# Kernel tuning notes

Hardware: AMD Instinct MI355X
Metric: run time of the kernel (lower is better)

Reference implementation:

```python
import jax, jax.numpy as jnp
import numpy as np
import math

N, E = 1000, 128000
IN_DIM, HID, OUT_DIM = 256, 512, 16
L, H = 6, 8
C = HID // H  # 64, TransformerConv out_channels per head
EDGE_DIM = 32
MAX_LEN = 1000


def _pe(max_len, d_model):
    pos = np.arange(max_len)[:, None].astype(np.float32)
    div = np.exp(np.arange(0, d_model, 2).astype(np.float32) * (-math.log(10000.0) / d_model))
    pe = np.zeros((max_len, d_model), dtype=np.float32)
    pe[:, 0::2] = np.sin(pos * div)
    pe[:, 1::2] = np.cos(pos * div)
    return jnp.asarray(pe)


def setup_inputs() -> dict:
    key = jax.random.key(0)
    ks = jax.random.split(key, 32)
    g = lambda k, shape, fan_in: jax.random.normal(k, shape, jnp.float32) / jnp.sqrt(jnp.float32(fan_in))
    inp = {
        "x": jax.random.normal(ks[0], (N, IN_DIM), jnp.float32),
        "edge_index": jax.random.randint(ks[1], (2, E), 0, N, jnp.int64 if jax.config.jax_enable_x64 else jnp.int32),
        "edge_attr": jax.random.uniform(ks[2], (E, 4), jnp.float32),
        "embed_w": g(ks[3], (IN_DIM, HID), IN_DIM),
        "embed_b": jnp.zeros((HID,), jnp.float32),
        "pe": _pe(MAX_LEN, HID),
        "ee_w1": g(ks[4], (4, 16), 4), "ee_b1": jnp.zeros((16,), jnp.float32),
        "ee_w2": g(ks[5], (16, EDGE_DIM), 16), "ee_b2": jnp.zeros((EDGE_DIM,), jnp.float32),
        "q_w": g(ks[6], (L, HID, HID), HID), "q_b": jnp.zeros((L, HID), jnp.float32),
        "k_w": g(ks[7], (L, HID, HID), HID), "k_b": jnp.zeros((L, HID), jnp.float32),
        "v_w": g(ks[8], (L, HID, HID), HID), "v_b": jnp.zeros((L, HID), jnp.float32),
        "e_w": g(ks[9], (L, EDGE_DIM, HID), EDGE_DIM),
        "skip_w": g(ks[10], (L, HID, HID), HID), "skip_b": jnp.zeros((L, HID), jnp.float32),
        "ln_g": jnp.ones((L, HID), jnp.float32), "ln_b": jnp.zeros((L, HID), jnp.float32),
        "dom_w": g(ks[11], (HID, 16), HID), "dom_b": jnp.zeros((16,), jnp.float32),
        "cls_w1": g(ks[12], (HID + 16, HID // 2), HID + 16), "cls_b1": jnp.zeros((HID // 2,), jnp.float32),
        "cls_w2": g(ks[13], (HID // 2, OUT_DIM), HID // 2), "cls_b2": jnp.zeros((OUT_DIM,), jnp.float32),
    }
    return inp


def _layer_norm(x, g, b, eps=1e-5):
    mu = jnp.mean(x, axis=-1, keepdims=True)
    var = jnp.var(x, axis=-1, keepdims=True)
    return (x - mu) * jax.lax.rsqrt(var + eps) * g + b


def _forward(x, edge_index, edge_attr, embed_w, embed_b, pe, ee_w1, ee_b1, ee_w2, ee_b2,
             q_w, q_b, k_w, k_b, v_w, v_b, e_w, skip_w, skip_b, ln_g, ln_b,
             dom_w, dom_b, cls_w1, cls_b1, cls_w2, cls_b2):
    n = x.shape[0]
    h = x @ embed_w + embed_b
    h = h + pe[:n]
    # edge encoder: 4 -> 16 -> 32
    ef = jax.nn.relu(edge_attr @ ee_w1 + ee_b1) @ ee_w2 + ee_b2  # [E, 32]
    src, tgt = edge_index[0], edge_index[1]
    scale = 1.0 / math.sqrt(C)
    for l in range(L):
        res = h
        q = (h @ q_w[l] + q_b[l]).reshape(n, H, C)
        k = (h @ k_w[l] + k_b[l]).reshape(n, H, C)
        v = (h @ v_w[l] + v_b[l]).reshape(n, H, C)
        e = (ef @ e_w[l]).reshape(-1, H, C)            # [E, H, C], lin_edge has no bias
        kj = k[src] + e                                 # gather + edge bias
        score = jnp.sum(q[tgt] * kj, axis=-1) * scale   # [E, H]
        # segment softmax over incoming edges of each target node
        m = jax.ops.segment_max(score, tgt, num_segments=n)     # [N, H]
        al = jnp.exp(score - m[tgt])
        den = jax.ops.segment_sum(al, tgt, num_segments=n)      # [N, H]
        al = al / den[tgt]
        msg = (v[src] + e) * al[:, :, None]             # [E, H, C]
        out = jax.ops.segment_sum(msg, tgt, num_segments=n).reshape(n, HID)
        out = out + h @ skip_w[l] + skip_b[l]           # root_weight skip
        h = _layer_norm(out + res, ln_g[l], ln_b[l])
    dom = h @ dom_w + dom_b                             # [N, 16]
    comb = jnp.concatenate([h, dom], axis=-1)
    hid = jax.nn.relu(comb @ cls_w1 + cls_b1)
    return hid @ cls_w2 + cls_b2


def reference(x, edge_index, edge_attr, embed_w, embed_b, pe, ee_w1, ee_b1, ee_w2, ee_b2,
              q_w, q_b, k_w, k_b, v_w, v_b, e_w, skip_w, skip_b, ln_g, ln_b,
              dom_w, dom_b, cls_w1, cls_b1, cls_w2, cls_b2):
    return _forward(x, edge_index, edge_attr, embed_w, embed_b, pe, ee_w1, ee_b1, ee_w2, ee_b2,
                    q_w, q_b, k_w, k_b, v_w, v_b, e_w, skip_w, skip_b, ln_g, ln_b,
                    dom_w, dom_b, cls_w1, cls_b1, cls_w2, cls_b2)
```

## Files before the change

kernel.cpp:

```cpp
#include <hip/hip_runtime.h>
#include <hip/hip_bf16.h>
#include <cstdint>
#include <cstddef>

#define NN 1000
#define EE 128000
#define LAYERS 6
#define SCALE 0.125f
#define MAXDEG 320

typedef __attribute__((ext_vector_type(4))) float f32x4;
typedef __attribute__((ext_vector_type(8))) short short8v;

static __device__ __forceinline__ unsigned short f2bf(float x){
    unsigned int u = __float_as_uint(x);
    unsigned int lsb = (u >> 16) & 1u;
    u += 0x7fffu + lsb;
    return (unsigned short)(u >> 16);
}
static __device__ __forceinline__ float bf2f(unsigned short u){
    return __uint_as_float(((unsigned int)u) << 16);
}

__global__ void zero_counts(int* cnt){
    cnt[threadIdx.x] = 0;
}

__global__ void hist_kernel(const int* __restrict__ tgt, int* cnt){
    int e = blockIdx.x*256 + threadIdx.x;
    if (e < EE) atomicAdd(&cnt[tgt[e]], 1);
}

__global__ void scan_kernel(const int* __restrict__ cnt, int* offs, int* cursor){
    __shared__ int s[1024];
    int tid = threadIdx.x;
    s[tid] = (tid < NN) ? cnt[tid] : 0;
    __syncthreads();
    for (int st = 1; st < 1024; st <<= 1){
        int v = (tid >= st) ? s[tid-st] : 0;
        __syncthreads();
        s[tid] += v;
        __syncthreads();
    }
    int excl = (tid == 0) ? 0 : s[tid-1];
    if (tid < NN){ offs[tid] = excl; cursor[tid] = excl; }
    if (tid == 0) offs[NN] = s[NN-1];
}

__global__ void scatter_kernel(const int* __restrict__ src, const int* __restrict__ tgt,
                               int* cursor, int* ssrc, int* epos){
    int e = blockIdx.x*256 + threadIdx.x;
    if (e < EE){
        int t = tgt[e];
        int pos = atomicAdd(&cursor[t], 1);
        ssrc[pos] = src[e];
        epos[e] = pos;
    }
}

__global__ __launch_bounds__(256) void edge_enc(
    const float* __restrict__ edge_attr,
    const float* __restrict__ w1, const float* __restrict__ b1,
    const float* __restrict__ w2, const float* __restrict__ b2,
    const int* __restrict__ epos,
    unsigned short* __restrict__ efs)
{
    __shared__ float w1s[64], b1s[16], w2s[512], b2s[32];
    int tid = threadIdx.x;
    if (tid < 64) w1s[tid] = w1[tid];
    if (tid < 16) b1s[tid] = b1[tid];
    if (tid < 32) b2s[tid] = b2[tid];
    w2s[tid] = w2[tid];
    w2s[tid+256] = w2[tid+256];
    __syncthreads();
    int e = blockIdx.x*256 + tid;
    if (e >= EE) return;
    float4 av = *(const float4*)(edge_attr + (size_t)e*4);
    float hd[16];
    #pragma unroll
    for (int i = 0; i < 16; i++){
        float v = av.x*w1s[i] + av.y*w1s[16+i] + av.z*w1s[32+i] + av.w*w1s[48+i] + b1s[i];
        hd[i] = fmaxf(v, 0.f);
    }
    unsigned short* op = efs + (size_t)epos[e]*32;
    #pragma unroll
    for (int k4 = 0; k4 < 8; k4++){
        ushort4 ub;
        float v0 = b2s[k4*4+0], v1 = b2s[k4*4+1], v2 = b2s[k4*4+2], v3 = b2s[k4*4+3];
        #pragma unroll
        for (int i = 0; i < 16; i++){
            float hv = hd[i];
            v0 += hv*w2s[i*32 + k4*4+0];
            v1 += hv*w2s[i*32 + k4*4+1];
            v2 += hv*w2s[i*32 + k4*4+2];
            v3 += hv*w2s[i*32 + k4*4+3];
        }
        ub.x = f2bf(v0); ub.y = f2bf(v1); ub.z = f2bf(v2); ub.w = f2bf(v3);
        *(ushort4*)(op + k4*4) = ub;
    }
}

__global__ __launch_bounds__(256) void convert_x(const float* __restrict__ x, unsigned short* __restrict__ xb){
    int row = blockIdx.x;
    int c = threadIdx.x;
    xb[(size_t)row*256 + c] = (row < NN) ? f2bf(x[(size_t)row*256 + c]) : (unsigned short)0;
}

__global__ __launch_bounds__(256) void tconv(const float* __restrict__ src, unsigned short* __restrict__ dst,
                                             int Kk, int Nn){
    int tn = blockIdx.x, tk = blockIdx.y;
    __shared__ float ts[32][33];
    int tid = threadIdx.x;
    int r = tid >> 3, c0 = (tid & 7)*4;
    float4 v = *(const float4*)(src + (size_t)(tk*32 + r)*Nn + tn*32 + c0);
    ts[r][c0+0] = v.x; ts[r][c0+1] = v.y; ts[r][c0+2] = v.z; ts[r][c0+3] = v.w;
    __syncthreads();
    ushort4 o;
    o.x = f2bf(ts[c0+0][r]); o.y = f2bf(ts[c0+1][r]);
    o.z = f2bf(ts[c0+2][r]); o.w = f2bf(ts[c0+3][r]);
    *(ushort4*)(dst + (size_t)(tn*32 + r)*Kk + tk*32 + c0) = o;
}

__global__ __launch_bounds__(256) void tconv24(
    const float* __restrict__ Wq, const float* __restrict__ Wk,
    const float* __restrict__ Wv, const float* __restrict__ Ws,
    unsigned short* __restrict__ Wt)
{
    int bid = blockIdx.x;
    int mm = bid >> 8;
    int tile = bid & 255;
    int tk = tile >> 4, tn = tile & 15;
    int l = mm >> 2, m = mm & 3;
    const float* W = ((m==0)?Wq:(m==1)?Wk:(m==2)?Wv:Ws) + (size_t)l*512*512;
    unsigned short* dst = Wt + (size_t)mm*512*512;
    __shared__ float ts[32][33];
    int tid = threadIdx.x;
    int r = tid >> 3, c0 = (tid & 7)*4;
    float4 v = *(const float4*)(W + (size_t)(tk*32 + r)*512 + tn*32 + c0);
    ts[r][c0+0] = v.x; ts[r][c0+1] = v.y; ts[r][c0+2] = v.z; ts[r][c0+3] = v.w;
    __syncthreads();
    ushort4 o;
    o.x = f2bf(ts[c0+0][r]); o.y = f2bf(ts[c0+1][r]);
    o.z = f2bf(ts[c0+2][r]); o.w = f2bf(ts[c0+3][r]);
    *(ushort4*)(dst + (size_t)(tn*32 + r)*512 + tk*32 + c0) = o;
}

__global__ __launch_bounds__(256) void gemm_embed_mfma(
    const unsigned short* __restrict__ xb,
    const unsigned short* __restrict__ ewt,
    const float* __restrict__ bias, const float* __restrict__ pe,
    float* __restrict__ C, unsigned short* __restrict__ hb)
{
    int bid = blockIdx.x;
    int mt = bid >> 2, nt = bid & 3;
    int row0 = mt*64, col0 = nt*128;

    __shared__ __align__(16) unsigned short As[64*40];
    __shared__ __align__(16) unsigned short Bs[128*40];

    int tid = threadIdx.x;
    int wid = tid >> 6, l = tid & 63;
    int wm = wid >> 1, wn = wid & 1;

    f32x4 acc[2][4] = {};
    int ar = tid >> 2, akq = tid & 3;
    for (int k0 = 0; k0 < 256; k0 += 32){
        *(uint4*)&As[ar*40 + akq*8]      = *(const uint4*)&xb[(size_t)(row0+ar)*256 + k0 + akq*8];
        *(uint4*)&Bs[ar*40 + akq*8]      = *(const uint4*)&ewt[(size_t)(col0+ar)*256 + k0 + akq*8];
        *(uint4*)&Bs[(ar+64)*40 + akq*8] = *(const uint4*)&ewt[(size_t)(col0+ar+64)*256 + k0 + akq*8];
        __syncthreads();
        short8v a0 = *(const short8v*)&As[(wm*32 + (l&15))*40 + (l>>4)*8];
        short8v a1 = *(const short8v*)&As[(wm*32 + 16 + (l&15))*40 + (l>>4)*8];
        #pragma unroll
        for (int nj = 0; nj < 4; nj++){
            short8v b = *(const short8v*)&Bs[(wn*64 + nj*16 + (l&15))*40 + (l>>4)*8];
            acc[0][nj] = __builtin_amdgcn_mfma_f32_16x16x32_bf16(a0, b, acc[0][nj], 0, 0, 0);
            acc[1][nj] = __builtin_amdgcn_mfma_f32_16x16x32_bf16(a1, b, acc[1][nj], 0, 0, 0);
        }
        __syncthreads();
    }
    int rbase = (l >> 4)*4, cl = l & 15;
    #pragma unroll
    for (int mi = 0; mi < 2; mi++)
        #pragma unroll
        for (int nj = 0; nj < 4; nj++)
            #pragma unroll
            for (int r = 0; r < 4; r++){
                int grow = row0 + wm*32 + mi*16 + rbase + r;
                int gcol = col0 + wn*64 + nj*16 + cl;
                if (grow < NN){
                    float v = acc[mi][nj][r] + bias[gcol] + pe[(size_t)grow*512 + gcol];
                    C[(size_t)grow*512 + gcol] = v;
                    hb[(size_t)grow*512 + gcol] = f2bf(v);
                }
            }
}

__global__ __launch_bounds__(256) void gemm_qkvs_mfma(
    const unsigned short* __restrict__ hb,
    const unsigned short* __restrict__ Wt,
    const float* __restrict__ qb, const float* __restrict__ kb,
    const float* __restrict__ vb, const float* __restrict__ sb,
    float* __restrict__ Q, unsigned short* __restrict__ K16,
    unsigned short* __restrict__ V16, float* __restrict__ S)
{
    int bid = blockIdx.x;
    int mat = bid >> 7;
    int rem = bid & 127;
    int mt = rem >> 3, nt = rem & 7;
    int row0 = mt*64, col0 = nt*64;
    const unsigned short* W = Wt + (size_t)mat*512*512;
    const float* bias = (mat==0)?qb:(mat==1)?kb:(mat==2)?vb:sb;

    __shared__ __align__(16) unsigned short As[64*72];
    __shared__ __align__(16) unsigned short Bs[64*72];

    int tid = threadIdx.x;
    int wid = tid >> 6, l = tid & 63;
    int wm = wid >> 1, wn = wid & 1;

    f32x4 acc[2][2] = {};
    int lr = tid >> 2;
    int lc = (tid & 3)*2;
    const unsigned short* ga = hb + (size_t)(row0+lr)*512 + lc*8;
    const unsigned short* gb = W  + (size_t)(col0+lr)*512 + lc*8;

    uint4 ra0 = *(const uint4*)(ga);
    uint4 ra1 = *(const uint4*)(ga + 8);
    uint4 rb0 = *(const uint4*)(gb);
    uint4 rb1 = *(const uint4*)(gb + 8);

    for (int k0 = 0; k0 < 512; k0 += 64){
        __syncthreads();
        *(uint4*)&As[lr*72 + lc*8]     = ra0;
        *(uint4*)&As[lr*72 + lc*8 + 8] = ra1;
        *(uint4*)&Bs[lr*72 + lc*8]     = rb0;
        *(uint4*)&Bs[lr*72 + lc*8 + 8] = rb1;
        __syncthreads();
        if (k0 + 64 < 512){
            ra0 = *(const uint4*)(ga + k0 + 64);
            ra1 = *(const uint4*)(ga + k0 + 72);
            rb0 = *(const uint4*)(gb + k0 + 64);
            rb1 = *(const uint4*)(gb + k0 + 72);
        }
        #pragma unroll
        for (int ks = 0; ks < 2; ks++){
            short8v a0 = *(const short8v*)&As[(wm*32 + (l&15))*72      + ks*32 + (l>>4)*8];
            short8v a1 = *(const short8v*)&As[(wm*32 + 16 + (l&15))*72 + ks*32 + (l>>4)*8];
            short8v b0 = *(const short8v*)&Bs[(wn*32 + (l&15))*72      + ks*32 + (l>>4)*8];
            short8v b1 = *(const short8v*)&Bs[(wn*32 + 16 + (l&15))*72 + ks*32 + (l>>4)*8];
            acc[0][0] = __builtin_amdgcn_mfma_f32_16x16x32_bf16(a0, b0, acc[0][0], 0, 0, 0);
            acc[0][1] = __builtin_amdgcn_mfma_f32_16x16x32_bf16(a0, b1, acc[0][1], 0, 0, 0);
            acc[1][0] = __builtin_amdgcn_mfma_f32_16x16x32_bf16(a1, b0, acc[1][0], 0, 0, 0);
            acc[1][1] = __builtin_amdgcn_mfma_f32_16x16x32_bf16(a1, b1, acc[1][1], 0, 0, 0);
        }
    }
    int rbase = (l >> 4)*4, cl = l & 15;
    #pragma unroll
    for (int mi = 0; mi < 2; mi++)
        #pragma unroll
        for (int nj = 0; nj < 2; nj++)
            #pragma unroll
            for (int r = 0; r < 4; r++){
                int grow = row0 + wm*32 + mi*16 + rbase + r;
                int gcol = col0 + wn*32 + nj*16 + cl;
                if (grow < NN){
                    float v = acc[mi][nj][r] + bias[gcol];
                    if (mat == 0)      Q[(size_t)grow*512 + gcol] = v;
                    else if (mat == 1) K16[(size_t)grow*512 + gcol] = f2bf(v);
                    else if (mat == 2) V16[(size_t)grow*512 + gcol] = f2bf(v);
                    else               S[(size_t)grow*512 + gcol] = v;
                }
            }
}

__global__ __launch_bounds__(512) void attn_layer(
    const float* __restrict__ hcur,
    const float* __restrict__ Qm, const unsigned short* __restrict__ Km,
    const unsigned short* __restrict__ Vm, const float* __restrict__ SKm,
    const unsigned short* __restrict__ efs, const float* __restrict__ e_w_l,
    const float* __restrict__ ln_g_l, const float* __restrict__ ln_b_l,
    const int* __restrict__ ssrc, const int* __restrict__ offs,
    float* __restrict__ hnext, unsigned short* __restrict__ hbn)
{
    int tid = threadIdx.x;
    int t = blockIdx.x;

    __shared__ float q_s[8*68];
    __shared__ float qe_s[8*36];
    __shared__ float sc_s[MAXDEG*8];
    __shared__ int   src_s[MAXDEG];
    __shared__ float pv_s[2048];
    __shared__ float pe_s[512];
    __shared__ float s_s[256];
    __shared__ float red[64], red2[64];
    __shared__ float m_s[8], d_s[8];

    q_s[(tid>>6)*68 + (tid&63)] = Qm[(size_t)t*512 + tid];
    __syncthreads();
    if (tid < 256){
        int hh = tid>>5, dd = tid&31;
        const float* wrow = e_w_l + (size_t)dd*512 + hh*64;
        const float* qh = q_s + hh*68;
        float a = 0.f;
        #pragma unroll
        for (int c = 0; c < 64; c++) a += qh[c]*wrow[c];
        qe_s[hh*36 + dd] = a;
    }
    int start = offs[t], deg = offs[t+1] - start;
    __syncthreads();

    int cw = tid >> 5, l = tid & 31;
    int h = l >> 2, sub = l & 3;
    const float4* qp4  = (const float4*)(q_s + h*68 + sub*16);
    const float4* qep4 = (const float4*)(qe_s + h*36 + sub*8);
    float4 qa0 = qp4[0], qa1 = qp4[1], qa2 = qp4[2], qa3 = qp4[3];
    float4 qe0 = qep4[0], qe1 = qep4[1];
    float lmax = -1e30f;
    for (int i = cw; i < deg; i += 16){
        int s = ssrc[start + i];
        if (l == 0) src_s[i] = s;
        const unsigned short* kr = Km + (size_t)s*512 + l*16;
        short8v k0 = *(const short8v*)(kr);
        short8v k1 = *(const short8v*)(kr + 8);
        short8v ev = *(const short8v*)(efs + (size_t)(start+i)*32 + sub*8);
        float p;
        p  = qa0.x*bf2f((unsigned short)k0[0]) + qa0.y*bf2f((unsigned short)k0[1])
           + qa0.z*bf2f((unsigned short)k0[2]) + qa0.w*bf2f((unsigned short)k0[3]);
        p += qa1.x*bf2f((unsigned short)k0[4]) + qa1.y*bf2f((unsigned short)k0[5])
           + qa1.z*bf2f((unsigned short)k0[6]) + qa1.w*bf2f((unsigned short)k0[7]);
        p += qa2.x*bf2f((unsigned short)k1[0]) + qa2.y*bf2f((unsigned short)k1[1])
           + qa2.z*bf2f((unsigned short)k1[2]) + qa2.w*bf2f((unsigned short)k1[3]);
        p += qa3.x*bf2f((unsigned short)k1[4]) + qa3.y*bf2f((unsigned short)k1[5])
           + qa3.z*bf2f((unsigned short)k1[6]) + qa3.w*bf2f((unsigned short)k1[7]);
        p += qe0.x*bf2f((unsigned short)ev[0]) + qe0.y*bf2f((unsigned short)ev[1])
           + qe0.z*bf2f((unsigned short)ev[2]) + qe0.w*bf2f((unsigned short)ev[3]);
        p += qe1.x*bf2f((unsigned short)ev[4]) + qe1.y*bf2f((unsigned short)ev[5])
           + qe1.z*bf2f((unsigned short)ev[6]) + qe1.w*bf2f((unsigned short)ev[7]);
        p += __shfl_xor(p, 1);
        p += __shfl_xor(p, 2);
        p *= SCALE;
        lmax = fmaxf(lmax, p);
        if (sub == 0) sc_s[i*8 + h] = p;
    }
    lmax = fmaxf(lmax, __shfl_xor(lmax, 32));
    if (((tid & 63) < 32) && sub == 0) red[(tid>>6)*8 + h] = lmax;
    __syncthreads();
    if (tid < 8){
        float m = red[tid];
        #pragma unroll
        for (int w = 1; w < 8; w++) m = fmaxf(m, red[w*8 + tid]);
        m_s[tid] = m;
    }
    __syncthreads();

    {
        int he = tid & 7, ie = tid >> 3;
        float mh = m_s[he];
        float den = 0.f;
        for (int i = ie; i < deg; i += 64){
            float al = __expf(sc_s[i*8 + he] - mh);
            sc_s[i*8 + he] = al;
            den += al;
        }
        den += __shfl_xor(den, 8);
        den += __shfl_xor(den, 16);
        den += __shfl_xor(den, 32);
        if ((tid & 63) < 8) red2[(tid>>6)*8 + (tid & 7)] = den;
    }
    __syncthreads();
    if (tid < 8){
        float d = 0.f;
        #pragma unroll
        for (int w = 0; w < 8; w++) d += red2[w*8 + tid];
        d_s[tid] = d;
    }
    __syncthreads();

    {
        int c4 = tid & 127, g = tid >> 7;
        int h2 = c4 >> 4;
        float4 acc = make_float4(0.f, 0.f, 0.f, 0.f);
        #pragma unroll 4
        for (int i = g; i < deg; i += 4){
            int s = src_s[i];
            float al = sc_s[i*8 + h2];
            ushort4 v = *(const ushort4*)(Vm + (size_t)s*512 + c4*4);
            acc.x += al*bf2f(v.x); acc.y += al*bf2f(v.y);
            acc.z += al*bf2f(v.z); acc.w += al*bf2f(v.w);
        }
        *(float4*)&pv_s[g*512 + c4*4] = acc;
    }
    {
        int c2 = tid & 255, g2 = tid >> 8;
        int h3 = c2 >> 5, dd3 = c2 & 31;
        float accE = 0.f;
        #pragma unroll 8
        for (int i = g2; i < deg; i += 2){
            float al = sc_s[i*8 + h3];
            accE += al * bf2f(efs[(size_t)(start+i)*32 + dd3]);
        }
        pe_s[g2*256 + c2] = accE;
    }
    __syncthreads();
    if (tid < 256){
        float dv = d_s[tid>>5];
        float invd = (dv > 0.f) ? 1.f/dv : 0.f;
        s_s[tid] = (pe_s[tid] + pe_s[256+tid]) * invd;
    }
    __syncthreads();

    int c = tid;
    int hh2 = c >> 6;
    float dv = d_s[hh2];
    float invd = (dv > 0.f) ? 1.f/dv : 0.f;
    float vtot = pv_s[c] + pv_s[512+c] + pv_s[1024+c] + pv_s[1536+c];
    float r = vtot * invd;
    float oe = 0.f;
    const float* sp = s_s + hh2*32;
    #pragma unroll
    for (int d = 0; d < 32; d++) oe += sp[d]*e_w_l[(size_t)d*512 + c];
    float x = r + oe + SKm[(size_t)t*512 + c] + hcur[(size_t)t*512 + c];

    int wv = tid >> 6, ln = tid & 63;
    float sA = x, sB = x*x;
    #pragma unroll
    for (int m2 = 1; m2 <= 32; m2 <<= 1){
        sA += __shfl_xor(sA, m2);
        sB += __shfl_xor(sB, m2);
    }
    if (ln == 0){ red[wv] = sA; red2[wv] = sB; }
    __syncthreads();
    float tot = 0.f, tot2 = 0.f;
    #pragma unroll
    for (int w = 0; w < 8; w++){ tot += red[w]; tot2 += red2[w]; }
    float mu  = tot*(1.f/512.f);
    float var = tot2*(1.f/512.f) - mu*mu;
    float rstd = rsqrtf(var + 1e-5f);
    float y = (x - mu)*rstd*ln_g_l[c] + ln_b_l[c];
    hnext[(size_t)t*512 + c] = y;
    hbn[(size_t)t*512 + c]   = f2bf(y);
}

__global__ __launch_bounds__(256) void final_head(
    const float* __restrict__ hin,
    const float* __restrict__ dom_w, const float* __restrict__ dom_b,
    const float* __restrict__ w1, const float* __restrict__ b1,
    const float* __restrict__ w2, const float* __restrict__ b2,
    float* __restrict__ out)
{
    int tid = threadIdx.x, t = blockIdx.x;
    __shared__ float h_s[512];
    __shared__ float dom_s[16];
    __shared__ float hid_s[256];
    __shared__ float red[256];
    h_s[tid]     = hin[(size_t)t*512 + tid];
    h_s[tid+256] = hin[(size_t)t*512 + 256 + tid];
    __syncthreads();
    if (tid < 16){
        float a = dom_b[tid];
        for (int i = 0; i < 512; i++) a += h_s[i]*dom_w[i*16 + tid];
        dom_s[tid] = a;
    }
    __syncthreads();
    float acc = b1[tid];
    for (int i = 0; i < 512; i++) acc += h_s[i]*w1[(size_t)i*256 + tid];
    #pragma unroll
    for (int i = 0; i < 16; i++) acc += dom_s[i]*w1[(size_t)(512+i)*256 + tid];
    hid_s[tid] = fmaxf(acc, 0.f);
    __syncthreads();
    int o = tid & 15, g = tid >> 4;
    float p = 0.f;
    #pragma unroll
    for (int j = 0; j < 16; j++) p += hid_s[g*16 + j]*w2[(g*16 + j)*16 + o];
    red[tid] = p;
    __syncthreads();
    if (tid < 16){
        float s2 = b2[tid];
        for (int gg = 0; gg < 16; gg++) s2 += red[gg*16 + tid];
        out[(size_t)t*16 + tid] = s2;
    }
}

extern "C" void kernel_launch(void* const* d_in, const int* in_sizes, int n_in,
                              void* d_out, int out_size, void* d_ws, size_t ws_size,
                              hipStream_t stream)
{
    const float* x       = (const float*)d_in[0];
    const int*   eidx    = (const int*)  d_in[1];
    const float* eattr   = (const float*)d_in[2];
    const float* embed_w = (const float*)d_in[3];
    const float* embed_b = (const float*)d_in[4];
    const float* pe      = (const float*)d_in[5];
    const float* ee_w1   = (const float*)d_in[6];
    const float* ee_b1   = (const float*)d_in[7];
    const float* ee_w2   = (const float*)d_in[8];
    const float* ee_b2   = (const float*)d_in[9];
    const float* q_w     = (const float*)d_in[10];
    const float* q_b     = (const float*)d_in[11];
    const float* k_w     = (const float*)d_in[12];
    const float* k_b     = (const float*)d_in[13];
    const float* v_w     = (const float*)d_in[14];
    const float* v_b     = (const float*)d_in[15];
    const float* e_w     = (const float*)d_in[16];
    const float* skip_w  = (const float*)d_in[17];
    const float* skip_b  = (const float*)d_in[18];
    const float* ln_g    = (const float*)d_in[19];
    const float* ln_b    = (const float*)d_in[20];
    const float* dom_w   = (const float*)d_in[21];
    const float* dom_b   = (const float*)d_in[22];
    const float* cls_w1  = (const float*)d_in[23];
    const float* cls_b1  = (const float*)d_in[24];
    const float* cls_w2  = (const float*)d_in[25];
    const float* cls_b2  = (const float*)d_in[26];
    float* out = (float*)d_out;

    float* ws = (float*)d_ws;
    size_t o = 0;
    float* h0    = ws + o; o += (size_t)512*NN;
    float* h1    = ws + o; o += (size_t)512*NN;
    float* Qb    = ws + o; o += (size_t)512*NN;
    float* Sb    = ws + o; o += (size_t)512*NN;
    unsigned short* Kb16 = (unsigned short*)(ws + o); o += (size_t)1024*512/2;
    unsigned short* Vb16 = (unsigned short*)(ws + o); o += (size_t)1024*512/2;
    unsigned short* efs  = (unsigned short*)(ws + o); o += (size_t)EE*32/2;
    unsigned short* hb   = (unsigned short*)(ws + o); o += (size_t)1024*512/2;
    unsigned short* xb   = (unsigned short*)(ws + o); o += (size_t)1024*256/2;
    unsigned short* ewt  = (unsigned short*)(ws + o); o += (size_t)512*256/2;
    unsigned short* Wtb  = (unsigned short*)(ws + o); o += (size_t)24*512*512/2;
    int* cnt    = (int*)(ws + o); o += 1024;
    int* offs   = (int*)(ws + o); o += 1024;
    int* cursor = (int*)(ws + o); o += 1024;
    int* ssrc   = (int*)(ws + o); o += EE;
    int* epos   = (int*)(ws + o); o += EE;

    const int* srcp = eidx;
    const int* tgtp = eidx + EE;

    zero_counts<<<1, 1024, 0, stream>>>(cnt);
    hist_kernel<<<EE/256, 256, 0, stream>>>(tgtp, cnt);
    scan_kernel<<<1, 1024, 0, stream>>>(cnt, offs, cursor);
    scatter_kernel<<<EE/256, 256, 0, stream>>>(srcp, tgtp, cursor, ssrc, epos);
    edge_enc<<<EE/256, 256, 0, stream>>>(eattr, ee_w1, ee_b1, ee_w2, ee_b2, epos, efs);
    convert_x<<<1024, 256, 0, stream>>>(x, xb);
    tconv<<<dim3(512/32, 256/32), 256, 0, stream>>>(embed_w, ewt, 256, 512);
    tconv24<<<24*256, 256, 0, stream>>>(q_w, k_w, v_w, skip_w, Wtb);
    gemm_embed_mfma<<<64, 256, 0, stream>>>(xb, ewt, embed_b, pe, h0, hb);

    float* hc = h0;
    float* hn = h1;
    for (int l = 0; l < LAYERS; l++){
        gemm_qkvs_mfma<<<512, 256, 0, stream>>>(
            hb, Wtb + (size_t)l*4*512*512,
            q_b + (size_t)l*512, k_b + (size_t)l*512,
            v_b + (size_t)l*512, skip_b + (size_t)l*512,
            Qb, Kb16, Vb16, Sb);
        attn_layer<<<NN, 512, 0, stream>>>(
            hc, Qb, Kb16, Vb16, Sb, efs, e_w + (size_t)l*32*512,
            ln_g + (size_t)l*512, ln_b + (size_t)l*512,
            ssrc, offs, hn, hb);
        float* tmp = hc; hc = hn; hn = tmp;
    }
    final_head<<<NN, 256, 0, stream>>>(hc, dom_w, dom_b, cls_w1, cls_b1, cls_w2, cls_b2, out);
}
```

Baseline: 581.1 us.

## Split attention per node across two head-group blocks and fuse weight conversions

```diff
diff --git a/kernel.cpp b/kernel.cpp
--- a/kernel.cpp
+++ b/kernel.cpp
@@ -100,49 +100,47 @@
     }
 }
 
-__global__ __launch_bounds__(256) void convert_x(const float* __restrict__ x, unsigned short* __restrict__ xb){
-    int row = blockIdx.x;
-    int c = threadIdx.x;
-    xb[(size_t)row*256 + c] = (row < NN) ? f2bf(x[(size_t)row*256 + c]) : (unsigned short)0;
-}
-
-__global__ __launch_bounds__(256) void tconv(const float* __restrict__ src, unsigned short* __restrict__ dst,
-                                             int Kk, int Nn){
-    int tn = blockIdx.x, tk = blockIdx.y;
-    __shared__ float ts[32][33];
-    int tid = threadIdx.x;
-    int r = tid >> 3, c0 = (tid & 7)*4;
-    float4 v = *(const float4*)(src + (size_t)(tk*32 + r)*Nn + tn*32 + c0);
-    ts[r][c0+0] = v.x; ts[r][c0+1] = v.y; ts[r][c0+2] = v.z; ts[r][c0+3] = v.w;
-    __syncthreads();
-    ushort4 o;
-    o.x = f2bf(ts[c0+0][r]); o.y = f2bf(ts[c0+1][r]);
-    o.z = f2bf(ts[c0+2][r]); o.w = f2bf(ts[c0+3][r]);
-    *(ushort4*)(dst + (size_t)(tn*32 + r)*Kk + tk*32 + c0) = o;
-}
-
-__global__ __launch_bounds__(256) void tconv24(
+__global__ __launch_bounds__(256) void convert_all(
     const float* __restrict__ Wq, const float* __restrict__ Wk,
     const float* __restrict__ Wv, const float* __restrict__ Ws,
-    unsigned short* __restrict__ Wt)
+    const float* __restrict__ embed_w, const float* __restrict__ x,
+    unsigned short* __restrict__ Wt, unsigned short* __restrict__ ewt,
+    unsigned short* __restrict__ xb)
 {
     int bid = blockIdx.x;
-    int mm = bid >> 8;
-    int tile = bid & 255;
-    int tk = tile >> 4, tn = tile & 15;
-    int l = mm >> 2, m = mm & 3;
-    const float* W = ((m==0)?Wq:(m==1)?Wk:(m==2)?Wv:Ws) + (size_t)l*512*512;
-    unsigned short* dst = Wt + (size_t)mm*512*512;
-    __shared__ float ts[32][33];
     int tid = threadIdx.x;
-    int r = tid >> 3, c0 = (tid & 7)*4;
-    float4 v = *(const float4*)(W + (size_t)(tk*32 + r)*512 + tn*32 + c0);
-    ts[r][c0+0] = v.x; ts[r][c0+1] = v.y; ts[r][c0+2] = v.z; ts[r][c0+3] = v.w;
-    __syncthreads();
-    ushort4 o;
-    o.x = f2bf(ts[c0+0][r]); o.y = f2bf(ts[c0+1][r]);
-    o.z = f2bf(ts[c0+2][r]); o.w = f2bf(ts[c0+3][r]);
-    *(ushort4*)(dst + (size_t)(tn*32 + r)*512 + tk*32 + c0) = o;
+    if (bid < 6144){
+        int mm = bid >> 8;
+        int tile = bid & 255;
+        int tk = tile >> 4, tn = tile & 15;
+        int l = mm >> 2, m = mm & 3;
+        const float* W = ((m==0)?Wq:(m==1)?Wk:(m==2)?Wv:Ws) + (size_t)l*512*512;
+        unsigned short* dst = Wt + (size_t)mm*512*512;
+        __shared__ float ts[32][33];
+        int r = tid >> 3, c0 = (tid & 7)*4;
+        float4 v = *(const float4*)(W + (size_t)(tk*32 + r)*512 + tn*32 + c0);
+        ts[r][c0+0] = v.x; ts[r][c0+1] = v.y; ts[r][c0+2] = v.z; ts[r][c0+3] = v.w;
+        __syncthreads();
+        ushort4 o;
+        o.x = f2bf(ts[c0+0][r]); o.y = f2bf(ts[c0+1][r]);
+        o.z = f2bf(ts[c0+2][r]); o.w = f2bf(ts[c0+3][r]);
+        *(ushort4*)(dst + (size_t)(tn*32 + r)*512 + tk*32 + c0) = o;
+    } else if (bid < 6144 + 128){
+        int tile = bid - 6144;
+        int tn = tile & 15, tk = tile >> 4;
+        __shared__ float ts2[32][33];
+        int r = tid >> 3, c0 = (tid & 7)*4;
+        float4 v = *(const float4*)(embed_w + (size_t)(tk*32 + r)*512 + tn*32 + c0);
+        ts2[r][c0+0] = v.x; ts2[r][c0+1] = v.y; ts2[r][c0+2] = v.z; ts2[r][c0+3] = v.w;
+        __syncthreads();
+        ushort4 o;
+        o.x = f2bf(ts2[c0+0][r]); o.y = f2bf(ts2[c0+1][r]);
+        o.z = f2bf(ts2[c0+2][r]); o.w = f2bf(ts2[c0+3][r]);
+        *(ushort4*)(ewt + (size_t)(tn*32 + r)*256 + tk*32 + c0) = o;
+    } else {
+        int row = bid - 6144 - 128;
+        xb[(size_t)row*256 + tid] = (row < NN) ? f2bf(x[(size_t)row*256 + tid]) : (unsigned short)0;
+    }
 }
 
 __global__ __launch_bounds__(256) void gemm_embed_mfma(
@@ -274,172 +272,174 @@
             }
 }
 
-__global__ __launch_bounds__(512) void attn_layer(
-    const float* __restrict__ hcur,
+__global__ __launch_bounds__(256) void attn_h4(
     const float* __restrict__ Qm, const unsigned short* __restrict__ Km,
-    const unsigned short* __restrict__ Vm, const float* __restrict__ SKm,
+    const unsigned short* __restrict__ Vm,
     const unsigned short* __restrict__ efs, const float* __restrict__ e_w_l,
-    const float* __restrict__ ln_g_l, const float* __restrict__ ln_b_l,
     const int* __restrict__ ssrc, const int* __restrict__ offs,
-    float* __restrict__ hnext, unsigned short* __restrict__ hbn)
+    float* __restrict__ x_pre)
 {
     int tid = threadIdx.x;
-    int t = blockIdx.x;
-
-    __shared__ float q_s[8*68];
-    __shared__ float qe_s[8*36];
-    __shared__ float sc_s[MAXDEG*8];
+    int b = blockIdx.x;
+    int t = b >> 1;
+    int hh0 = (b & 1)*4;
+
+    __shared__ float q_s[4*68];
+    __shared__ float qe_s[4*36];
+    __shared__ float sc_s[MAXDEG*4];
     __shared__ int   src_s[MAXDEG];
-    __shared__ float pv_s[2048];
-    __shared__ float pe_s[512];
-    __shared__ float s_s[256];
-    __shared__ float red[64], red2[64];
-    __shared__ float m_s[8], d_s[8];
-
-    q_s[(tid>>6)*68 + (tid&63)] = Qm[(size_t)t*512 + tid];
-    __syncthreads();
-    if (tid < 256){
-        int hh = tid>>5, dd = tid&31;
-        const float* wrow = e_w_l + (size_t)dd*512 + hh*64;
-        const float* qh = q_s + hh*68;
+    __shared__ float pv_s[4*256];
+    __shared__ float pe_s[4*128];
+    __shared__ float s_s[128];
+    __shared__ float red[16], red2[16];
+    __shared__ float m_s[4], d_s[4];
+
+    q_s[(tid>>6)*68 + (tid&63)] = Qm[(size_t)t*512 + hh0*64 + tid];
+    __syncthreads();
+    if (tid < 128){
+        int h = tid >> 5, d = tid & 31;
+        const float* wrow = e_w_l + (size_t)d*512 + (hh0+h)*64;
+        const float* qh = q_s + h*68;
         float a = 0.f;
         #pragma unroll
         for (int c = 0; c < 64; c++) a += qh[c]*wrow[c];
-        qe_s[hh*36 + dd] = a;
+        qe_s[h*36 + d] = a;
     }
     int start = offs[t], deg = offs[t+1] - start;
     __syncthreads();
 
     int cw = tid >> 5, l = tid & 31;
-    int h = l >> 2, sub = l & 3;
-    const float4* qp4  = (const float4*)(q_s + h*68 + sub*16);
-    const float4* qep4 = (const float4*)(qe_s + h*36 + sub*8);
-    float4 qa0 = qp4[0], qa1 = qp4[1], qa2 = qp4[2], qa3 = qp4[3];
-    float4 qe0 = qep4[0], qe1 = qep4[1];
+    int h = l >> 3, sub = l & 7;
+    const float4* qp4  = (const float4*)(q_s + h*68 + sub*8);
+    float4 qa0 = qp4[0], qa1 = qp4[1];
+    float4 qev = *(const float4*)(qe_s + h*36 + sub*4);
     float lmax = -1e30f;
-    for (int i = cw; i < deg; i += 16){
+    #pragma unroll 2
+    for (int i = cw; i < deg; i += 8){
         int s = ssrc[start + i];
         if (l == 0) src_s[i] = s;
-        const unsigned short* kr = Km + (size_t)s*512 + l*16;
-        short8v k0 = *(const short8v*)(kr);
-        short8v k1 = *(const short8v*)(kr + 8);
-        short8v ev = *(const short8v*)(efs + (size_t)(start+i)*32 + sub*8);
+        short8v kv = *(const short8v*)(Km + (size_t)s*512 + (hh0 + h)*64 + sub*8);
+        ushort4 ev = *(const ushort4*)(efs + (size_t)(start+i)*32 + sub*4);
         float p;
-        p  = qa0.x*bf2f((unsigned short)k0[0]) + qa0.y*bf2f((unsigned short)k0[1])
-           + qa0.z*bf2f((unsigned short)k0[2]) + qa0.w*bf2f((unsigned short)k0[3]);
-        p += qa1.x*bf2f((unsigned short)k0[4]) + qa1.y*bf2f((unsigned short)k0[5])
-           + qa1.z*bf2f((unsigned short)k0[6]) + qa1.w*bf2f((unsigned short)k0[7]);
-        p += qa2.x*bf2f((unsigned short)k1[0]) + qa2.y*bf2f((unsigned short)k1[1])
-           + qa2.z*bf2f((unsigned short)k1[2]) + qa2.w*bf2f((unsigned short)k1[3]);
-        p += qa3.x*bf2f((unsigned short)k1[4]) + qa3.y*bf2f((unsigned short)k1[5])
-           + qa3.z*bf2f((unsigned short)k1[6]) + qa3.w*bf2f((unsigned short)k1[7]);
-        p += qe0.x*bf2f((unsigned short)ev[0]) + qe0.y*bf2f((unsigned short)ev[1])
-           + qe0.z*bf2f((unsigned short)ev[2]) + qe0.w*bf2f((unsigned short)ev[3]);
-        p += qe1.x*bf2f((unsigned short)ev[4]) + qe1.y*bf2f((unsigned short)ev[5])
-           + qe1.z*bf2f((unsigned short)ev[6]) + qe1.w*bf2f((unsigned short)ev[7]);
+        p  = qa0.x*bf2f((unsigned short)kv[0]) + qa0.y*bf2f((unsigned short)kv[1])
+           + qa0.z*bf2f((unsigned short)kv[2]) + qa0.w*bf2f((unsigned short)kv[3]);
+        p += qa1.x*bf2f((unsigned short)kv[4]) + qa1.y*bf2f((unsigned short)kv[5])
+           + qa1.z*bf2f((unsigned short)kv[6]) + qa1.w*bf2f((unsigned short)kv[7]);
+        p += qev.x*bf2f(ev.x) + qev.y*bf2f(ev.y)
+           + qev.z*bf2f(ev.z) + qev.w*bf2f(ev.w);
         p += __shfl_xor(p, 1);
         p += __shfl_xor(p, 2);
+        p += __shfl_xor(p, 4);
         p *= SCALE;
         lmax = fmaxf(lmax, p);
-        if (sub == 0) sc_s[i*8 + h] = p;
+        if (sub == 0) sc_s[i*4 + h] = p;
     }
     lmax = fmaxf(lmax, __shfl_xor(lmax, 32));
-    if (((tid & 63) < 32) && sub == 0) red[(tid>>6)*8 + h] = lmax;
-    __syncthreads();
-    if (tid < 8){
-        float m = red[tid];
-        #pragma unroll
-        for (int w = 1; w < 8; w++) m = fmaxf(m, red[w*8 + tid]);
+    {
+        int wl = tid & 63;
+        if (wl < 32 && (wl & 7) == 0) red[(tid>>6)*4 + (wl>>3)] = lmax;
+    }
+    __syncthreads();
+    if (tid < 4){
+        float m = fmaxf(fmaxf(red[tid], red[4+tid]), fmaxf(red[8+tid], red[12+tid]));
         m_s[tid] = m;
     }
     __syncthreads();
 
     {
-        int he = tid & 7, ie = tid >> 3;
+        int he = tid & 3, ie = tid >> 2;
         float mh = m_s[he];
         float den = 0.f;
         for (int i = ie; i < deg; i += 64){
-            float al = __expf(sc_s[i*8 + he] - mh);
-            sc_s[i*8 + he] = al;
+            float al = __expf(sc_s[i*4 + he] - mh);
+            sc_s[i*4 + he] = al;
             den += al;
         }
+        den += __shfl_xor(den, 4);
         den += __shfl_xor(den, 8);
         den += __shfl_xor(den, 16);
         den += __shfl_xor(den, 32);
-        if ((tid & 63) < 8) red2[(tid>>6)*8 + (tid & 7)] = den;
-    }
-    __syncthreads();
-    if (tid < 8){
-        float d = 0.f;
-        #pragma unroll
-        for (int w = 0; w < 8; w++) d += red2[w*8 + tid];
-        d_s[tid] = d;
-    }
+        if ((tid & 63) < 4) red2[(tid>>6)*4 + (tid & 3)] = den;
+    }
+    __syncthreads();
+    if (tid < 4) d_s[tid] = red2[tid] + red2[4+tid] + red2[8+tid] + red2[12+tid];
     __syncthreads();
 
     {
-        int c4 = tid & 127, g = tid >> 7;
+        int g = tid >> 6, c4 = tid & 63;
         int h2 = c4 >> 4;
-        float4 acc = make_float4(0.f, 0.f, 0.f, 0.f);
+        int dp = (c4 & 15)*2;
+        float4 accV = make_float4(0.f,0.f,0.f,0.f);
+        float2 accE = make_float2(0.f,0.f);
         #pragma unroll 4
         for (int i = g; i < deg; i += 4){
             int s = src_s[i];
-            float al = sc_s[i*8 + h2];
-            ushort4 v = *(const ushort4*)(Vm + (size_t)s*512 + c4*4);
-            acc.x += al*bf2f(v.x); acc.y += al*bf2f(v.y);
-            acc.z += al*bf2f(v.z); acc.w += al*bf2f(v.w);
+            float al = sc_s[i*4 + h2];
+            ushort4 v = *(const ushort4*)(Vm + (size_t)s*512 + hh0*64 + c4*4);
+            unsigned int e2 = *(const unsigned int*)(efs + (size_t)(start+i)*32 + dp);
+            accV.x += al*bf2f(v.x); accV.y += al*bf2f(v.y);
+            accV.z += al*bf2f(v.z); accV.w += al*bf2f(v.w);
+            accE.x += al*bf2f((unsigned short)(e2 & 0xffffu));
+            accE.y += al*bf2f((unsigned short)(e2 >> 16));
         }
-        *(float4*)&pv_s[g*512 + c4*4] = acc;
-    }
-    {
-        int c2 = tid & 255, g2 = tid >> 8;
-        int h3 = c2 >> 5, dd3 = c2 & 31;
-        float accE = 0.f;
-        #pragma unroll 8
-        for (int i = g2; i < deg; i += 2){
-            float al = sc_s[i*8 + h3];
-            accE += al * bf2f(efs[(size_t)(start+i)*32 + dd3]);
-        }
-        pe_s[g2*256 + c2] = accE;
-    }
-    __syncthreads();
-    if (tid < 256){
-        float dv = d_s[tid>>5];
+        *(float4*)&pv_s[g*256 + c4*4] = accV;
+        *(float2*)&pe_s[g*128 + c4*2] = accE;
+    }
+    __syncthreads();
+    if (tid < 128){
+        int h3 = tid >> 5, d = tid & 31;
+        int c4s = h3*16 + (d >> 1), comp = d & 1;
+        float dv = d_s[h3];
         float invd = (dv > 0.f) ? 1.f/dv : 0.f;
-        s_s[tid] = (pe_s[tid] + pe_s[256+tid]) * invd;
+        float ssum = pe_s[c4s*2+comp] + pe_s[128 + c4s*2+comp]
+                   + pe_s[256 + c4s*2+comp] + pe_s[384 + c4s*2+comp];
+        s_s[h3*32 + d] = ssum * invd;
     }
     __syncthreads();
 
     int c = tid;
-    int hh2 = c >> 6;
-    float dv = d_s[hh2];
+    int hh = c >> 6;
+    float dv = d_s[hh];
     float invd = (dv > 0.f) ? 1.f/dv : 0.f;
-    float vtot = pv_s[c] + pv_s[512+c] + pv_s[1024+c] + pv_s[1536+c];
+    float vtot = pv_s[c] + pv_s[256+c] + pv_s[512+c] + pv_s[768+c];
     float r = vtot * invd;
     float oe = 0.f;
-    const float* sp = s_s + hh2*32;
-    #pragma unroll
-    for (int d = 0; d < 32; d++) oe += sp[d]*e_w_l[(size_t)d*512 + c];
-    float x = r + oe + SKm[(size_t)t*512 + c] + hcur[(size_t)t*512 + c];
-
+    const float* sp = s_s + hh*32;
+    #pragma unroll
+    for (int d = 0; d < 32; d++) oe += sp[d]*e_w_l[(size_t)d*512 + hh0*64 + c];
+    x_pre[(size_t)t*512 + hh0*64 + c] = r + oe;
+}
+
+__global__ __launch_bounds__(256) void ln_skip(
+    const float* __restrict__ x_pre, const float* __restrict__ SKm,
+    const float* __restrict__ hcur,
+    const float* __restrict__ ln_g_l, const float* __restrict__ ln_b_l,
+    float* __restrict__ hnext, unsigned short* __restrict__ hbn)
+{
+    int tid = threadIdx.x, t = blockIdx.x;
+    __shared__ float red[4], red2[4];
+    float x0 = x_pre[(size_t)t*512 + tid]       + SKm[(size_t)t*512 + tid]       + hcur[(size_t)t*512 + tid];
+    float x1 = x_pre[(size_t)t*512 + 256 + tid] + SKm[(size_t)t*512 + 256 + tid] + hcur[(size_t)t*512 + 256 + tid];
+    float sA = x0 + x1, sB = x0*x0 + x1*x1;
+    #pragma unroll
+    for (int m = 1; m <= 32; m <<= 1){
+        sA += __shfl_xor(sA, m);
+        sB += __shfl_xor(sB, m);
+    }
     int wv = tid >> 6, ln = tid & 63;
-    float sA = x, sB = x*x;
-    #pragma unroll
-    for (int m2 = 1; m2 <= 32; m2 <<= 1){
-        sA += __shfl_xor(sA, m2);
-        sB += __shfl_xor(sB, m2);
-    }
     if (ln == 0){ red[wv] = sA; red2[wv] = sB; }
     __syncthreads();
-    float tot = 0.f, tot2 = 0.f;
-    #pragma unroll
-    for (int w = 0; w < 8; w++){ tot += red[w]; tot2 += red2[w]; }
+    float tot  = red[0] + red[1] + red[2] + red[3];
+    float tot2 = red2[0] + red2[1] + red2[2] + red2[3];
     float mu  = tot*(1.f/512.f);
     float var = tot2*(1.f/512.f) - mu*mu;
     float rstd = rsqrtf(var + 1e-5f);
-    float y = (x - mu)*rstd*ln_g_l[c] + ln_b_l[c];
-    hnext[(size_t)t*512 + c] = y;
-    hbn[(size_t)t*512 + c]   = f2bf(y);
+    float y0 = (x0 - mu)*rstd*ln_g_l[tid]     + ln_b_l[tid];
+    float y1 = (x1 - mu)*rstd*ln_g_l[256+tid] + ln_b_l[256+tid];
+    hnext[(size_t)t*512 + tid]       = y0;
+    hnext[(size_t)t*512 + 256 + tid] = y1;
+    hbn[(size_t)t*512 + tid]       = f2bf(y0);
+    hbn[(size_t)t*512 + 256 + tid] = f2bf(y1);
 }
 
 __global__ __launch_bounds__(256) void final_head(
@@ -521,6 +521,7 @@
     float* h1    = ws + o; o += (size_t)512*NN;
     float* Qb    = ws + o; o += (size_t)512*NN;
     float* Sb    = ws + o; o += (size_t)512*NN;
+    float* xpre  = ws + o; o += (size_t)512*NN;
     unsigned short* Kb16 = (unsigned short*)(ws + o); o += (size_t)1024*512/2;
     unsigned short* Vb16 = (unsigned short*)(ws + o); o += (size_t)1024*512/2;
     unsigned short* efs  = (unsigned short*)(ws + o); o += (size_t)EE*32/2;
@@ -542,9 +543,7 @@
     scan_kernel<<<1, 1024, 0, stream>>>(cnt, offs, cursor);
     scatter_kernel<<<EE/256, 256, 0, stream>>>(srcp, tgtp, cursor, ssrc, epos);
     edge_enc<<<EE/256, 256, 0, stream>>>(eattr, ee_w1, ee_b1, ee_w2, ee_b2, epos, efs);
-    convert_x<<<1024, 256, 0, stream>>>(x, xb);
-    tconv<<<dim3(512/32, 256/32), 256, 0, stream>>>(embed_w, ewt, 256, 512);
-    tconv24<<<24*256, 256, 0, stream>>>(q_w, k_w, v_w, skip_w, Wtb);
+    convert_all<<<6144 + 128 + 1024, 256, 0, stream>>>(q_w, k_w, v_w, skip_w, embed_w, x, Wtb, ewt, xb);
     gemm_embed_mfma<<<64, 256, 0, stream>>>(xb, ewt, embed_b, pe, h0, hb);
 
     float* hc = h0;
@@ -555,10 +554,13 @@
             q_b + (size_t)l*512, k_b + (size_t)l*512,
             v_b + (size_t)l*512, skip_b + (size_t)l*512,
             Qb, Kb16, Vb16, Sb);
-        attn_layer<<<NN, 512, 0, stream>>>(
-            hc, Qb, Kb16, Vb16, Sb, efs, e_w + (size_t)l*32*512,
+        attn_h4<<<2*NN, 256, 0, stream>>>(
+            Qb, Kb16, Vb16, efs, e_w + (size_t)l*32*512,
+            ssrc, offs, xpre);
+        ln_skip<<<NN, 256, 0, stream>>>(
+            xpre, Sb, hc,
             ln_g + (size_t)l*512, ln_b + (size_t)l*512,
-            ssrc, offs, hn, hb);
+            hn, hb);
         float* tmp = hc; hc = hn; hn = tmp;
     }
     final_head<<<NN, 256, 0, stream>>>(hc, dom_w, dom_b, cls_w1, cls_b1, cls_w2, cls_b2, out);
```

Result: faster. 551.7 us (-5.1%).
